# Kernel optimization log

Measured on AMD Instinct MI355X. Metric: run time of the kernel, lower is better.

Reference implementation:

```python
import jax, jax.numpy as jnp
import numpy as np

EPS = 1e-9
NUM_HEADS = 16
D = 1024      # input_dim == hidden_dim
B, S = 2, 2048


def layer_norm(x, scale, shift):
    mu = x.mean(axis=-1, keepdims=True)
    # torch std is unbiased (ddof=1); eps added to std, not variance
    std = jnp.std(x, axis=-1, ddof=1, keepdims=True)
    return scale * (x - mu) / (std + EPS) + shift


def setup_inputs() -> dict:
    key = jax.random.key(0)
    ks = jax.random.split(key, 18)
    d, h = D, D
    w = lambda k, sh: jax.random.normal(k, sh, dtype=jnp.float32) * 0.02
    return {
        "inputs": jax.random.normal(ks[0], (B, S, d), dtype=jnp.float32),
        "ln1_scale": jax.random.normal(ks[1], (d,), dtype=jnp.float32),
        "ln1_shift": jax.random.normal(ks[2], (d,), dtype=jnp.float32),
        "Wq": w(ks[3], (d, h)), "bq": jnp.zeros((h,), jnp.float32),
        "Wk": w(ks[4], (d, h)), "bk": jnp.zeros((h,), jnp.float32),
        "Wv": w(ks[5], (d, h)), "bv": jnp.zeros((h,), jnp.float32),
        "Wo": w(ks[6], (h, d)), "bo": jnp.zeros((d,), jnp.float32),
        "W1": w(ks[7], (d, 4 * d)), "b1": jnp.zeros((4 * d,), jnp.float32),
        "W2": w(ks[8], (4 * d, d)), "b2": jnp.zeros((d,), jnp.float32),
        "ln2_scale": jax.random.normal(ks[9], (d,), dtype=jnp.float32),
        "ln2_shift": jax.random.normal(ks[10], (d,), dtype=jnp.float32),
    }


def mhsa(x, Wq, bq, Wk, bk, Wv, bv, Wo, bo):
    b, s, d = x.shape
    nh, dh = NUM_HEADS, D // NUM_HEADS
    q = (x @ Wq + bq).reshape(b, s, nh, dh).transpose(0, 2, 1, 3)  # b h s d
    k = (x @ Wk + bk).reshape(b, s, nh, dh).transpose(0, 2, 1, 3)
    v = (x @ Wv + bv).reshape(b, s, nh, dh).transpose(0, 2, 1, 3)
    scores = jnp.einsum("bhqd,bhkd->bhqk", q, k) / jnp.sqrt(jnp.float32(dh))
    causal = jnp.triu(jnp.ones((s, s), dtype=bool), k=1)  # mask above diagonal
    scores = jnp.where(causal, -jnp.inf, scores)
    p = jax.nn.softmax(scores, axis=-1)
    p = jnp.where(jnp.isnan(p), 0.0, p)  # NaN-fill as in original
    out = jnp.einsum("bhqk,bhkd->bhqd", p, v)
    out = out.transpose(0, 2, 1, 3).reshape(b, s, nh * dh)
    return out @ Wo + bo


def reference(inputs, ln1_scale, ln1_shift, Wq, bq, Wk, bk, Wv, bv, Wo, bo,
              W1, b1, W2, b2, ln2_scale, ln2_shift):
    o1 = layer_norm(inputs, ln1_scale, ln1_shift)
    o1 = mhsa(o1, Wq, bq, Wk, bk, Wv, bv, Wo, bo) + inputs
    o2 = layer_norm(o1, ln2_scale, ln2_shift)
    # NOTE: original adds the residual from the *normalized* tensor, not o1
    ffn = jax.nn.relu(o2 @ W1 + b1) @ W2 + b2
    return ffn + o2
```

## Files before the change

### kernel.cpp

```cpp
#include <hip/hip_runtime.h>
#include <hip/hip_bf16.h>
#include <math.h>

#define BB 2
#define SS 2048
#define DD 1024
#define HH 16
#define DH 64
#define NROW (BB*SS)
#define FFN (4*DD)

typedef __attribute__((ext_vector_type(8))) __bf16 bf16x8;
typedef __attribute__((ext_vector_type(4))) float f32x4;

__device__ __forceinline__ ushort f2b(float f) {
    union { float f; uint32_t u; } x; x.f = f;
    uint32_t r = x.u + 0x7FFF + ((x.u >> 16) & 1);
    return (ushort)(r >> 16);
}
__device__ __forceinline__ float b2f(ushort u) {
    union { uint32_t u; float f; } x; x.u = (uint32_t)u << 16;
    return x.f;
}

__global__ __launch_bounds__(256)
void ln_kernel(const float* __restrict__ x, const float* __restrict__ scale,
               const float* __restrict__ shift, ushort* __restrict__ y) {
    int row = blockIdx.x;
    const float* xr = x + (size_t)row * DD;
    ushort* yr = y + (size_t)row * DD;
    int t = threadIdx.x;
    float v[4];
    float s = 0.f, ss = 0.f;
#pragma unroll
    for (int i = 0; i < 4; ++i) {
        v[i] = xr[t + 256 * i];
        s += v[i];
        ss += v[i] * v[i];
    }
#pragma unroll
    for (int off = 32; off; off >>= 1) {
        s  += __shfl_xor(s, off);
        ss += __shfl_xor(ss, off);
    }
    __shared__ float red[8];
    int w = t >> 6;
    if ((t & 63) == 0) { red[w] = s; red[w + 4] = ss; }
    __syncthreads();
    float st  = red[0] + red[1] + red[2] + red[3];
    float sst = red[4] + red[5] + red[6] + red[7];
    float mu = st * (1.f / DD);
    float var = (sst - DD * mu * mu) * (1.f / (DD - 1));
    var = fmaxf(var, 0.f);
    float inv = 1.f / (sqrtf(var) + 1e-9f);
#pragma unroll
    for (int i = 0; i < 4; ++i) {
        int c = t + 256 * i;
        yr[c] = f2b(scale[c] * (v[i] - mu) * inv + shift[c]);
    }
}

__global__ __launch_bounds__(256)
void ln_res_kernel(const ushort* __restrict__ xa, const float* __restrict__ xb,
                   const float* __restrict__ scale, const float* __restrict__ shift,
                   ushort* __restrict__ yb) {
    int row = blockIdx.x;
    const ushort* ar = xa + (size_t)row * DD;
    const float* br = xb + (size_t)row * DD;
    ushort* ybr = yb + (size_t)row * DD;
    int t = threadIdx.x;
    float v[4];
    float s = 0.f, ss = 0.f;
#pragma unroll
    for (int i = 0; i < 4; ++i) {
        int c = t + 256 * i;
        v[i] = b2f(ar[c]) + br[c];
        s += v[i];
        ss += v[i] * v[i];
    }
#pragma unroll
    for (int off = 32; off; off >>= 1) {
        s  += __shfl_xor(s, off);
        ss += __shfl_xor(ss, off);
    }
    __shared__ float red[8];
    int w = t >> 6;
    if ((t & 63) == 0) { red[w] = s; red[w + 4] = ss; }
    __syncthreads();
    float st  = red[0] + red[1] + red[2] + red[3];
    float sst = red[4] + red[5] + red[6] + red[7];
    float mu = st * (1.f / DD);
    float var = (sst - DD * mu * mu) * (1.f / (DD - 1));
    var = fmaxf(var, 0.f);
    float inv = 1.f / (sqrtf(var) + 1e-9f);
#pragma unroll
    for (int i = 0; i < 4; ++i) {
        int c = t + 256 * i;
        ybr[c] = f2b(scale[c] * (v[i] - mu) * inv + shift[c]);
    }
}

__global__ __launch_bounds__(256)
void transpose_bf16_kernel(const float* __restrict__ W, ushort* __restrict__ Wt,
                           int K, int N) {
    __shared__ ushort tile[32][33];
    int tx = threadIdx.x & 31;
    int ty = threadIdx.x >> 5;
    int n0 = blockIdx.x * 32;
    int k0 = blockIdx.y * 32;
#pragma unroll
    for (int i = 0; i < 32; i += 8)
        tile[ty + i][tx] = f2b(W[(size_t)(k0 + ty + i) * N + n0 + tx]);
    __syncthreads();
#pragma unroll
    for (int i = 0; i < 32; i += 8)
        Wt[(size_t)(n0 + ty + i) * K + k0 + tx] = tile[tx][ty + i];
}

#define GBM 128
#define GBN 128
#define GBK 32

template <int MODE, bool BF16_OUT, int DEPTH>
__global__ __launch_bounds__(512)
void gemm_bf16_kernel(const ushort* __restrict__ A, const ushort* __restrict__ Wt,
                      const float* __restrict__ bias, const ushort* __restrict__ addsrc,
                      void* __restrict__ Cout, int M, int N, int K,
                      const float* __restrict__ bias2, const float* __restrict__ bias3,
                      void* __restrict__ out2, void* __restrict__ out3) {
    __shared__ ushort As[DEPTH][GBM * GBK];
    __shared__ ushort Bs[DEPTH][GBN * GBK];

    int tid = threadIdx.x;
    int lane = tid & 63;
    int wid = tid >> 6;
    int wr = wid >> 2, wc = wid & 3;

    int gx = gridDim.x;
    int nwg = gx * gridDim.y;
    int orig = blockIdx.y * gx + blockIdx.x;
    int q8 = nwg >> 3;
    int swz = (orig & 7) * q8 + (orig >> 3);
    int bx = swz % gx, by = swz / gx;

    int brow = by * GBM;
    int bcol = bx * GBN;

    int lrow = lane & 15;
    int kgrp = lane >> 4;

    f32x4 acc[4][2] = {};

    int srow = tid >> 2;
    int sgran = (tid & 3) ^ ((srow >> 1) & 3);

    auto stage = [&](int buf, int k0) {
        const char* ga = (const char*)A +
            ((size_t)(brow + srow) * K + k0) * 2 + sgran * 16;
        __builtin_amdgcn_global_load_lds(
            (const __attribute__((address_space(1))) uint32_t*)ga,
            (__attribute__((address_space(3))) uint32_t*)(&As[buf][0] + (wid * 16) * GBK),
            16, 0, 0);
        const char* gb = (const char*)Wt +
            ((size_t)(bcol + srow) * K + k0) * 2 + sgran * 16;
        __builtin_amdgcn_global_load_lds(
            (const __attribute__((address_space(1))) uint32_t*)gb,
            (__attribute__((address_space(3))) uint32_t*)(&Bs[buf][0] + (wid * 16) * GBK),
            16, 0, 0);
    };

    int nk = K / GBK;
    constexpr int PRE = DEPTH - 1;
#pragma unroll
    for (int s = 0; s < PRE; ++s)
        if (s < nk) stage(s, s * GBK);

    int cur = 0, stg = PRE;
    for (int t = 0; t < nk; ++t) {
        __builtin_amdgcn_sched_barrier(0);
        int rem = nk - 1 - t;
        if constexpr (DEPTH == 5) {
            if (rem >= 3)      asm volatile("s_waitcnt vmcnt(6)" ::: "memory");
            else if (rem == 2) asm volatile("s_waitcnt vmcnt(4)" ::: "memory");
            else if (rem == 1) asm volatile("s_waitcnt vmcnt(2)" ::: "memory");
            else               asm volatile("s_waitcnt vmcnt(0)" ::: "memory");
        } else {
            if (rem >= 1)      asm volatile("s_waitcnt vmcnt(2)" ::: "memory");
            else               asm volatile("s_waitcnt vmcnt(0)" ::: "memory");
        }
        asm volatile("s_barrier" ::: "memory");
        if (t + PRE < nk) stage(stg, (t + PRE) * GBK);

        bf16x8 afrag[4], bfrag[2];
#pragma unroll
        for (int mi = 0; mi < 4; ++mi) {
            int row = wr * 64 + mi * 16 + lrow;
            int gran = kgrp ^ ((row >> 1) & 3);
            afrag[mi] = *(const bf16x8*)((const char*)&As[cur][0] + row * 64 + gran * 16);
        }
#pragma unroll
        for (int ni = 0; ni < 2; ++ni) {
            int row = wc * 32 + ni * 16 + lrow;
            int gran = kgrp ^ ((row >> 1) & 3);
            bfrag[ni] = *(const bf16x8*)((const char*)&Bs[cur][0] + row * 64 + gran * 16);
        }
#pragma unroll
        for (int mi = 0; mi < 4; ++mi)
#pragma unroll
            for (int ni = 0; ni < 2; ++ni)
                acc[mi][ni] = __builtin_amdgcn_mfma_f32_16x16x32_bf16(
                    afrag[mi], bfrag[ni], acc[mi][ni], 0, 0, 0);

        cur = (cur == DEPTH - 1) ? 0 : cur + 1;
        stg = (stg == DEPTH - 1) ? 0 : stg + 1;
    }

    if (MODE == 3) {
        int which = bcol >> 10;
        const float* bs = which == 0 ? bias : (which == 1 ? bias2 : bias3);
#pragma unroll
        for (int ni = 0; ni < 2; ++ni) {
            int col = bcol + wc * 32 + ni * 16 + lrow;
            int lcol = col & 1023;
            float bsv = bs[lcol];
#pragma unroll
            for (int mi = 0; mi < 4; ++mi) {
                f32x4 a = acc[mi][ni];
#pragma unroll
                for (int j = 0; j < 4; ++j) {
                    int row = brow + wr * 64 + mi * 16 + kgrp * 4 + j;
                    float val = a[j] + bsv;
                    if (which == 2) {
                        size_t idx = (size_t)(row >> 11) * ((size_t)DD * SS)
                                   + (size_t)lcol * SS + (row & (SS - 1));
                        ((ushort*)out3)[idx] = f2b(val);
                    } else {
                        ushort* dst = which == 0 ? (ushort*)Cout : (ushort*)out2;
                        dst[(size_t)row * DD + lcol] = f2b(val);
                    }
                }
            }
        }
        return;
    }

#pragma unroll
    for (int ni = 0; ni < 2; ++ni) {
        int col = bcol + wc * 32 + ni * 16 + lrow;
        float bsv = bias[col];
#pragma unroll
        for (int mi = 0; mi < 4; ++mi) {
            f32x4 a = acc[mi][ni];
#pragma unroll
            for (int j = 0; j < 4; ++j) {
                int row = brow + wr * 64 + mi * 16 + kgrp * 4 + j;
                float val = a[j] + bsv;
                if (MODE == 1) val = fmaxf(val, 0.f);
                if (MODE == 2) val += b2f(addsrc[(size_t)row * N + col]);
                if (BF16_OUT)
                    ((ushort*)Cout)[(size_t)row * N + col] = f2b(val);
                else
                    ((float*)Cout)[(size_t)row * N + col] = val;
            }
        }
    }
}

__global__ __launch_bounds__(256)
void attn_mfma_kernel(const ushort* __restrict__ Qg, const ushort* __restrict__ Kg,
                      const ushort* __restrict__ Vtg, ushort* __restrict__ Og) {
    __shared__ ushort Qs[64 * 64];
    __shared__ ushort Ks[2][64 * 64];
    __shared__ ushort Vs[2][64 * 64];

    int tid = threadIdx.x;
    int lane = tid & 63;
    int wid = tid >> 6;
    int bh = blockIdx.x;
    int b = bh >> 4, h = bh & 15;
    int q0 = ((int)gridDim.y - 1 - (int)blockIdx.y) * 64;

    const ushort* Qbase = Qg + ((size_t)(b * SS + q0)) * DD + h * DH;
    const ushort* Kbase = Kg + ((size_t)(b * SS)) * DD + h * DH;
    const ushort* Vbase = Vtg + (size_t)bh * DH * SS;

    int r0 = wid * 16;
    int rr0 = r0 + (lane >> 3);
    int g0 = lane & 7;
    int g = lane >> 4;
    int lr = lane & 15;

    auto stageKV = [&](int buf, int k0) {
#pragma unroll
        for (int i = 0; i < 2; ++i) {
            int rr = rr0 + i * 8;
            int gg = g0 ^ (rr & 7);
            const ushort* srck = Kbase + (size_t)(k0 + rr) * DD + gg * 8;
            __builtin_amdgcn_global_load_lds(
                (const __attribute__((address_space(1))) uint32_t*)srck,
                (__attribute__((address_space(3))) uint32_t*)(&Ks[buf][0] + (r0 + i * 8) * 64),
                16, 0, 0);
            const ushort* srcv = Vbase + (size_t)rr * SS + k0 + gg * 8;
            __builtin_amdgcn_global_load_lds(
                (const __attribute__((address_space(1))) uint32_t*)srcv,
                (__attribute__((address_space(3))) uint32_t*)(&Vs[buf][0] + (r0 + i * 8) * 64),
                16, 0, 0);
        }
    };

    int nt = q0 / 64 + 1;

    {
#pragma unroll
        for (int i = 0; i < 2; ++i) {
            int rr = rr0 + i * 8;
            int gg = g0 ^ (rr & 7);
            const ushort* src = Qbase + (size_t)rr * DD + gg * 8;
            __builtin_amdgcn_global_load_lds(
                (const __attribute__((address_space(1))) uint32_t*)src,
                (__attribute__((address_space(3))) uint32_t*)(Qs + (r0 + i * 8) * 64),
                16, 0, 0);
        }
    }
    stageKV(0, 0);
    asm volatile("s_waitcnt vmcnt(4)" ::: "memory");

    bf16x8 aq[2];
    {
        int r = wid * 16 + lr;
#pragma unroll
        for (int ks = 0; ks < 2; ++ks) {
            int lg = ks * 4 + g;
            aq[ks] = *(const bf16x8*)((const char*)Qs + r * 128 + ((lg ^ (r & 7)) << 4));
        }
    }
    ushort* Ps = Qs;

    f32x4 oacc[4] = {};
    float m = -INFINITY, l = 0.f;
    int qa = q0 + wid * 16 + lr;

    int cur = 0;
    for (int t = 0; t < nt; ++t) {
        __builtin_amdgcn_sched_barrier(0);
        asm volatile("s_waitcnt vmcnt(0)" ::: "memory");
        asm volatile("s_barrier" ::: "memory");
        if (t + 1 < nt) stageKV(cur ^ 1, (t + 1) * 64);
        int k0 = t * 64;

        f32x4 sacc[4] = {};
        __builtin_amdgcn_s_setprio(1);
#pragma unroll
        for (int ni = 0; ni < 4; ++ni) {
            int r = ni * 16 + lr;
#pragma unroll
            for (int ks = 0; ks < 2; ++ks) {
                int lg = ks * 4 + g;
                bf16x8 bk = *(const bf16x8*)((const char*)&Ks[cur][0] + r * 128 + ((lg ^ (r & 7)) << 4));
                sacc[ni] = __builtin_amdgcn_mfma_f32_16x16x32_bf16(bk, aq[ks], sacc[ni], 0, 0, 0);
            }
        }
        __builtin_amdgcn_s_setprio(0);

        float sc[4][4];
#pragma unroll
        for (int ni = 0; ni < 4; ++ni)
#pragma unroll
            for (int j = 0; j < 4; ++j)
                sc[ni][j] = sacc[ni][j] * 0.125f;
        if (k0 == q0) {
#pragma unroll
            for (int ni = 0; ni < 4; ++ni) {
#pragma unroll
                for (int j = 0; j < 4; ++j) {
                    int key = q0 + ni * 16 + g * 4 + j;
                    if (key > qa) sc[ni][j] = -INFINITY;
                }
            }
        }

        float mx = sc[0][0];
#pragma unroll
        for (int ni = 0; ni < 4; ++ni)
#pragma unroll
            for (int j = 0; j < 4; ++j) mx = fmaxf(mx, sc[ni][j]);
        mx = fmaxf(mx, __shfl_xor(mx, 16));
        mx = fmaxf(mx, __shfl_xor(mx, 32));
        float mn = fmaxf(m, mx);
        float corr = __expf(m - mn);
        m = mn;
        float p[4][4];
        float rs = 0.f;
#pragma unroll
        for (int ni = 0; ni < 4; ++ni)
#pragma unroll
            for (int j = 0; j < 4; ++j) { p[ni][j] = __expf(sc[ni][j] - mn); rs += p[ni][j]; }
        rs += __shfl_xor(rs, 16);
        rs += __shfl_xor(rs, 32);
        l = l * corr + rs;

        float cj[4];
#pragma unroll
        for (int j = 0; j < 4; ++j)
            cj[j] = __shfl(corr, (lane & 48) | (g * 4 + j));
#pragma unroll
        for (int ni = 0; ni < 4; ++ni)
#pragma unroll
            for (int j = 0; j < 4; ++j) oacc[ni][j] *= cj[j];

        {
            int row = wid * 16 + lr;
#pragma unroll
            for (int ni = 0; ni < 4; ++ni) {
                ushort4 w4;
                w4.x = f2b(p[ni][0]); w4.y = f2b(p[ni][1]);
                w4.z = f2b(p[ni][2]); w4.w = f2b(p[ni][3]);
                int gran = (ni * 2 + (g >> 1)) ^ (row & 7);
                *(ushort4*)((char*)Ps + row * 128 + (gran << 4) + (g & 1) * 8) = w4;
            }
        }
        asm volatile("s_waitcnt lgkmcnt(0)" ::: "memory");

        bf16x8 ap[2];
        {
            int r = wid * 16 + lr;
#pragma unroll
            for (int ks = 0; ks < 2; ++ks) {
                int lg = ks * 4 + g;
                ap[ks] = *(const bf16x8*)((const char*)Ps + r * 128 + ((lg ^ (r & 7)) << 4));
            }
        }
        __builtin_amdgcn_s_setprio(1);
#pragma unroll
        for (int ni = 0; ni < 4; ++ni) {
            int r = ni * 16 + lr;
#pragma unroll
            for (int ks = 0; ks < 2; ++ks) {
                int lg = ks * 4 + g;
                bf16x8 bv = *(const bf16x8*)((const char*)&Vs[cur][0] + r * 128 + ((lg ^ (r & 7)) << 4));
                oacc[ni] = __builtin_amdgcn_mfma_f32_16x16x32_bf16(ap[ks], bv, oacc[ni], 0, 0, 0);
            }
        }
        __builtin_amdgcn_s_setprio(0);
        cur ^= 1;
    }

#pragma unroll
    for (int j = 0; j < 4; ++j) {
        float lj = __shfl(l, (lane & 48) | (g * 4 + j));
        float inv = 1.f / lj;
        int gr = q0 + wid * 16 + g * 4 + j;
#pragma unroll
        for (int ni = 0; ni < 4; ++ni) {
            int d = ni * 16 + lr;
            Og[((size_t)(b * SS + gr)) * DD + h * DH + d] = f2b(oacc[ni][j] * inv);
        }
    }
}

extern "C" void kernel_launch(void* const* d_in, const int* in_sizes, int n_in,
                              void* d_out, int out_size, void* d_ws, size_t ws_size,
                              hipStream_t stream) {
    const float* inputs    = (const float*)d_in[0];
    const float* ln1_scale = (const float*)d_in[1];
    const float* ln1_shift = (const float*)d_in[2];
    const float* Wq = (const float*)d_in[3];
    const float* bq = (const float*)d_in[4];
    const float* Wk = (const float*)d_in[5];
    const float* bk = (const float*)d_in[6];
    const float* Wv = (const float*)d_in[7];
    const float* bv = (const float*)d_in[8];
    const float* Wo = (const float*)d_in[9];
    const float* bo = (const float*)d_in[10];
    const float* W1 = (const float*)d_in[11];
    const float* b1 = (const float*)d_in[12];
    const float* W2 = (const float*)d_in[13];
    const float* b2 = (const float*)d_in[14];
    const float* ln2_scale = (const float*)d_in[15];
    const float* ln2_shift = (const float*)d_in[16];
    float* out = (float*)d_out;

    const size_t MB = 1024 * 1024;
    char* w = (char*)d_ws;
    ushort* q_b   = (ushort*)(w + 0 * MB);
    ushort* k_b   = (ushort*)(w + 8 * MB);
    ushort* vt_b  = (ushort*)(w + 16 * MB);
    ushort* att_b = (ushort*)(w + 24 * MB);
    ushort* proj_b= (ushort*)(w + 32 * MB);
    ushort* o2_b  = (ushort*)(w + 48 * MB);
    ushort* h1_b  = (ushort*)(w + 64 * MB);
    ushort* wq_t  = (ushort*)(w + 96 * MB);
    ushort* wk_t  = (ushort*)(w + 98 * MB);
    ushort* wv_t  = (ushort*)(w + 100 * MB);
    ushort* wo_t  = (ushort*)(w + 102 * MB);
    ushort* w1_t  = (ushort*)(w + 104 * MB);
    ushort* w2_t  = (ushort*)(w + 112 * MB);
    ushort* xn_b  = (ushort*)(w + 120 * MB);

    transpose_bf16_kernel<<<dim3(DD / 32, DD / 32), 256, 0, stream>>>(Wq, wq_t, DD, DD);
    transpose_bf16_kernel<<<dim3(DD / 32, DD / 32), 256, 0, stream>>>(Wk, wk_t, DD, DD);
    transpose_bf16_kernel<<<dim3(DD / 32, DD / 32), 256, 0, stream>>>(Wv, wv_t, DD, DD);
    transpose_bf16_kernel<<<dim3(DD / 32, DD / 32), 256, 0, stream>>>(Wo, wo_t, DD, DD);
    transpose_bf16_kernel<<<dim3(FFN / 32, DD / 32), 256, 0, stream>>>(W1, w1_t, DD, FFN);
    transpose_bf16_kernel<<<dim3(DD / 32, FFN / 32), 256, 0, stream>>>(W2, w2_t, FFN, DD);

    ln_kernel<<<NROW, 256, 0, stream>>>(inputs, ln1_scale, ln1_shift, xn_b);

    dim3 gqkv(3 * DD / GBN, NROW / GBM);
    gemm_bf16_kernel<3, true, 3><<<gqkv, 512, 0, stream>>>(
        xn_b, wq_t, bq, nullptr, q_b, NROW, 3 * DD, DD, bk, bv, k_b, vt_b);

    dim3 ga(BB * HH, SS / 64);
    attn_mfma_kernel<<<ga, 256, 0, stream>>>(q_b, k_b, vt_b, att_b);

    dim3 g1(DD / GBN, NROW / GBM);
    gemm_bf16_kernel<0, true, 5><<<g1, 512, 0, stream>>>(
        att_b, wo_t, bo, nullptr, proj_b, NROW, DD, DD, nullptr, nullptr, nullptr, nullptr);

    ln_res_kernel<<<NROW, 256, 0, stream>>>(proj_b, inputs, ln2_scale, ln2_shift, o2_b);

    dim3 g2(FFN / GBN, NROW / GBM);
    gemm_bf16_kernel<1, true, 3><<<g2, 512, 0, stream>>>(
        o2_b, w1_t, b1, nullptr, h1_b, NROW, FFN, DD, nullptr, nullptr, nullptr, nullptr);

    gemm_bf16_kernel<2, false, 5><<<g1, 512, 0, stream>>>(
        h1_b, w2_t, b2, o2_b, out, NROW, DD, FFN, nullptr, nullptr, nullptr, nullptr);
}
```

Measured before the change: 268.0 us.

## Split-K by two for Wo and FFN2 GEMMs with separate reduce kernels

The output-projection and second FFN GEMMs now run with a z-dimension of 2, each half computing over half of K and writing fp32 partials. Small elementwise kernels then sum the partials, add bias (and the residual for FFN2) and write the final outputs. The aim is to double the workgroup count for the N=1024 GEMMs to fill the GPU better. In exchange it adds extra fp32 partial-sum traffic and two additional kernel launches.

```diff
diff --git a/kernel.cpp b/kernel.cpp
--- a/kernel.cpp
+++ b/kernel.cpp
@@ -117,6 +117,40 @@
         Wt[(size_t)(n0 + ty + i) * K + k0 + tx] = tile[tx][ty + i];
 }
 
+__global__ __launch_bounds__(256)
+void reduce_wo_kernel(const float* __restrict__ p0, const float* __restrict__ p1,
+                      const float* __restrict__ bias, ushort* __restrict__ yb) {
+    int i = (blockIdx.x * 256 + threadIdx.x) * 4;
+    float4 a = *reinterpret_cast<const float4*>(p0 + i);
+    float4 b = *reinterpret_cast<const float4*>(p1 + i);
+    int c = i & (DD - 1);
+    float4 bs = *reinterpret_cast<const float4*>(bias + c);
+    ushort4 o;
+    o.x = f2b(a.x + b.x + bs.x);
+    o.y = f2b(a.y + b.y + bs.y);
+    o.z = f2b(a.z + b.z + bs.z);
+    o.w = f2b(a.w + b.w + bs.w);
+    *reinterpret_cast<ushort4*>(yb + i) = o;
+}
+
+__global__ __launch_bounds__(256)
+void reduce_ffn2_kernel(const float* __restrict__ p0, const float* __restrict__ p1,
+                        const float* __restrict__ bias, const ushort* __restrict__ res,
+                        float* __restrict__ out) {
+    int i = (blockIdx.x * 256 + threadIdx.x) * 4;
+    float4 a = *reinterpret_cast<const float4*>(p0 + i);
+    float4 b = *reinterpret_cast<const float4*>(p1 + i);
+    ushort4 r = *reinterpret_cast<const ushort4*>(res + i);
+    int c = i & (DD - 1);
+    float4 bs = *reinterpret_cast<const float4*>(bias + c);
+    float4 o;
+    o.x = a.x + b.x + bs.x + b2f(r.x);
+    o.y = a.y + b.y + bs.y + b2f(r.y);
+    o.z = a.z + b.z + bs.z + b2f(r.z);
+    o.w = a.w + b.w + bs.w + b2f(r.w);
+    *reinterpret_cast<float4*>(out + i) = o;
+}
+
 #define GBM 128
 #define GBN 128
 #define GBK 32
@@ -125,7 +159,7 @@
 __global__ __launch_bounds__(512)
 void gemm_bf16_kernel(const ushort* __restrict__ A, const ushort* __restrict__ Wt,
                       const float* __restrict__ bias, const ushort* __restrict__ addsrc,
-                      void* __restrict__ Cout, int M, int N, int K,
+                      void* __restrict__ Cout, int M, int N, int K, int lda,
                       const float* __restrict__ bias2, const float* __restrict__ bias3,
                       void* __restrict__ out2, void* __restrict__ out3) {
     __shared__ ushort As[DEPTH][GBM * GBK];
@@ -145,6 +179,7 @@
 
     int brow = by * GBM;
     int bcol = bx * GBN;
+    size_t koff = (size_t)blockIdx.z * K;
 
     int lrow = lane & 15;
     int kgrp = lane >> 4;
@@ -156,13 +191,13 @@
 
     auto stage = [&](int buf, int k0) {
         const char* ga = (const char*)A +
-            ((size_t)(brow + srow) * K + k0) * 2 + sgran * 16;
+            ((size_t)(brow + srow) * lda + koff + k0) * 2 + sgran * 16;
         __builtin_amdgcn_global_load_lds(
             (const __attribute__((address_space(1))) uint32_t*)ga,
             (__attribute__((address_space(3))) uint32_t*)(&As[buf][0] + (wid * 16) * GBK),
             16, 0, 0);
         const char* gb = (const char*)Wt +
-            ((size_t)(bcol + srow) * K + k0) * 2 + sgran * 16;
+            ((size_t)(bcol + srow) * lda + koff + k0) * 2 + sgran * 16;
         __builtin_amdgcn_global_load_lds(
             (const __attribute__((address_space(1))) uint32_t*)gb,
             (__attribute__((address_space(3))) uint32_t*)(&Bs[buf][0] + (wid * 16) * GBK),
@@ -244,6 +279,24 @@
         return;
     }
 
+    if (MODE == 4) {
+        float* dst = (float*)Cout + (size_t)blockIdx.z * ((size_t)M * N);
+#pragma unroll
+        for (int ni = 0; ni < 2; ++ni) {
+            int col = bcol + wc * 32 + ni * 16 + lrow;
+#pragma unroll
+            for (int mi = 0; mi < 4; ++mi) {
+                f32x4 a = acc[mi][ni];
+#pragma unroll
+                for (int j = 0; j < 4; ++j) {
+                    int row = brow + wr * 64 + mi * 16 + kgrp * 4 + j;
+                    dst[(size_t)row * N + col] = a[j];
+                }
+            }
+        }
+        return;
+    }
+
 #pragma unroll
     for (int ni = 0; ni < 2; ++ni) {
         int col = bcol + wc * 32 + ni * 16 + lrow;
@@ -256,7 +309,6 @@
                 int row = brow + wr * 64 + mi * 16 + kgrp * 4 + j;
                 float val = a[j] + bsv;
                 if (MODE == 1) val = fmaxf(val, 0.f);
-                if (MODE == 2) val += b2f(addsrc[(size_t)row * N + col]);
                 if (BF16_OUT)
                     ((ushort*)Cout)[(size_t)row * N + col] = f2b(val);
                 else
@@ -486,8 +538,10 @@
     ushort* k_b   = (ushort*)(w + 8 * MB);
     ushort* vt_b  = (ushort*)(w + 16 * MB);
     ushort* att_b = (ushort*)(w + 24 * MB);
-    ushort* proj_b= (ushort*)(w + 32 * MB);
-    ushort* o2_b  = (ushort*)(w + 48 * MB);
+    float*  pw    = (float*)(w + 32 * MB);
+    ushort* proj_b= (ushort*)(w + 0 * MB);
+    ushort* o2_b  = (ushort*)(w + 8 * MB);
+    float*  pf    = (float*)(w + 16 * MB);
     ushort* h1_b  = (ushort*)(w + 64 * MB);
     ushort* wq_t  = (ushort*)(w + 96 * MB);
     ushort* wk_t  = (ushort*)(w + 98 * MB);
@@ -506,23 +560,27 @@
 
     ln_kernel<<<NROW, 256, 0, stream>>>(inputs, ln1_scale, ln1_shift, xn_b);
 
-    dim3 gqkv(3 * DD / GBN, NROW / GBM);
+    dim3 gqkv(3 * DD / GBN, NROW / GBM, 1);
     gemm_bf16_kernel<3, true, 3><<<gqkv, 512, 0, stream>>>(
-        xn_b, wq_t, bq, nullptr, q_b, NROW, 3 * DD, DD, bk, bv, k_b, vt_b);
+        xn_b, wq_t, bq, nullptr, q_b, NROW, 3 * DD, DD, DD, bk, bv, k_b, vt_b);
 
     dim3 ga(BB * HH, SS / 64);
     attn_mfma_kernel<<<ga, 256, 0, stream>>>(q_b, k_b, vt_b, att_b);
 
-    dim3 g1(DD / GBN, NROW / GBM);
-    gemm_bf16_kernel<0, true, 5><<<g1, 512, 0, stream>>>(
-        att_b, wo_t, bo, nullptr, proj_b, NROW, DD, DD, nullptr, nullptr, nullptr, nullptr);
+    dim3 g1z(DD / GBN, NROW / GBM, 2);
+    gemm_bf16_kernel<4, false, 5><<<g1z, 512, 0, stream>>>(
+        att_b, wo_t, nullptr, nullptr, pw, NROW, DD, DD / 2, DD, nullptr, nullptr, nullptr, nullptr);
+    reduce_wo_kernel<<<(NROW * DD / 4) / 256, 256, 0, stream>>>(
+        pw, pw + (size_t)NROW * DD, bo, proj_b);
 
     ln_res_kernel<<<NROW, 256, 0, stream>>>(proj_b, inputs, ln2_scale, ln2_shift, o2_b);
 
-    dim3 g2(FFN / GBN, NROW / GBM);
+    dim3 g2(FFN / GBN, NROW / GBM, 1);
     gemm_bf16_kernel<1, true, 3><<<g2, 512, 0, stream>>>(
-        o2_b, w1_t, b1, nullptr, h1_b, NROW, FFN, DD, nullptr, nullptr, nullptr, nullptr);
-
-    gemm_bf16_kernel<2, false, 5><<<g1, 512, 0, stream>>>(
-        h1_b, w2_t, b2, o2_b, out, NROW, DD, FFN, nullptr, nullptr, nullptr, nullptr);
-}
+        o2_b, w1_t, b1, nullptr, h1_b, NROW, FFN, DD, DD, nullptr, nullptr, nullptr, nullptr);
+
+    gemm_bf16_kernel<4, false, 5><<<g1z, 512, 0, stream>>>(
+        h1_b, w2_t, nullptr, nullptr, pf, NROW, DD, FFN / 2, FFN, nullptr, nullptr, nullptr, nullptr);
+    reduce_ffn2_kernel<<<(NROW * DD / 4) / 256, 256, 0, stream>>>(
+        pf, pf + (size_t)NROW * DD, b2, o2_b, out);
+}
```

After: 257.0 us. 1.04x faster.
